# Optimization experiments

Hardware: AMD Instinct MI355X
Metric: run time of the kernel (lower is better)

Reference implementation:

```python
import jax, jax.numpy as jnp
import numpy as np

B, T, F_IN, H, L = 32, 2000, 80, 512, 2


def _ln(x, g, b, eps=1e-5):
    m = x.mean(-1, keepdims=True)
    v = x.var(-1, keepdims=True)
    return (x - m) / jnp.sqrt(v + eps) * g + b


def setup_inputs() -> dict:
    key = jax.random.key(0)
    ks = jax.random.split(key, 6)
    s = lambda k, shape, sc: jax.random.normal(k, shape, jnp.float32) * sc
    return {
        "x": s(ks[0], (B, T, F_IN), 1.0),
        "W_proj": s(ks[1], (F_IN, H), (1.0 / F_IN) ** 0.5),
        "b_proj": jnp.zeros((H,), jnp.float32),
        "ln1_g": jnp.ones((H,), jnp.float32),
        "ln1_b": jnp.zeros((H,), jnp.float32),
        "W_in": s(ks[2], (L, H, H), (1.0 / H) ** 0.5),
        "W_rec": s(ks[3], (L, H, H), (1.0 / H) ** 0.5),
        "b_rnn": jnp.zeros((L, H), jnp.float32),
        "tau_raw": jnp.ones((L, H), jnp.float32),
        "lno_g": jnp.ones((H,), jnp.float32),
        "lno_b": jnp.zeros((H,), jnp.float32),
    }


def _ltc_layer(x_tbh, W_i, W_r, b, tau_raw):
    # Liquid Time-Constant cell: tau*dh/dt = -h + tanh(Wx + Uh + b), dt = 1
    tau = jax.nn.softplus(tau_raw) + 0.1  # per-unit time constant, >0
    xz = jnp.einsum('tbf,fh->tbh', x_tbh, W_i) + b  # precompute input drive

    def step(h, xz_t):
        z = xz_t + h @ W_r
        h_new = h + (-h + jnp.tanh(z)) / tau
        return h_new, h_new

    h0 = jnp.zeros((x_tbh.shape[1], W_r.shape[0]), x_tbh.dtype)
    h_last, ys = jax.lax.scan(step, h0, xz)
    return ys, h_last


def reference(x, W_proj, b_proj, ln1_g, ln1_b, W_in, W_rec, b_rnn, tau_raw, lno_g, lno_b):
    # input projection: Linear -> LayerNorm -> GELU (dropout=0 in eval)
    h = jax.nn.gelu(_ln(x @ W_proj + b_proj, ln1_g, ln1_b), approximate=False)
    seq = jnp.transpose(h, (1, 0, 2))  # [T, B, H] for scan
    finals = []
    for l in range(W_in.shape[0]):
        seq, h_last = _ltc_layer(seq, W_in[l], W_rec[l], b_rnn[l], tau_raw[l])
        finals.append(h_last)
    encoded = _ln(jnp.transpose(seq, (1, 0, 2)), lno_g, lno_b)  # [B, T, H]
    hidden = jnp.stack(finals)  # [L, B, H]
    return encoded, hidden
```

## Files before the change

kernel.cpp:

```cpp
#include <hip/hip_runtime.h>
#include <math.h>

#define B_    32
#define T_    2000
#define FIN_  80
#define H_    512
#define ROWS_ (B_ * T_)
#define BTH_  ((size_t)ROWS_ * H_)
#define BH_   (B_ * H_)

typedef unsigned long long u64;

__global__ __launch_bounds__(256) void proj_ln_gelu(
    const float* __restrict__ x, const float* __restrict__ Wp,
    const float* __restrict__ bp, const float* __restrict__ g1,
    const float* __restrict__ be1, float* __restrict__ out)
{
  __shared__ float xs[16][84];
  __shared__ float pr[16][512];
  __shared__ float mv[16][2];
  const int tid = threadIdx.x;
  const int r0 = blockIdx.x * 16;

  for (int f = tid; f < 320; f += 256) {
    int rr = f / 20, c4 = (f % 20) * 4;
    int r = r0 + rr; int b = r & 31; int t = r >> 5;
    float4 v = *(const float4*)(x + ((size_t)(b * T_ + t)) * FIN_ + c4);
    xs[rr][c4+0] = v.x; xs[rr][c4+1] = v.y; xs[rr][c4+2] = v.z; xs[rr][c4+3] = v.w;
  }
  __syncthreads();

  const int j = tid;
  float acc0[16], acc1[16];
#pragma unroll
  for (int rr = 0; rr < 16; ++rr) { acc0[rr] = 0.f; acc1[rr] = 0.f; }

  for (int k4 = 0; k4 < 20; ++k4) {
    float w0[4], w1[4];
#pragma unroll
    for (int i = 0; i < 4; ++i) {
      w0[i] = Wp[(k4*4+i)*H_ + j];
      w1[i] = Wp[(k4*4+i)*H_ + j + 256];
    }
#pragma unroll
    for (int rr = 0; rr < 16; ++rr) {
      float4 xv = *(const float4*)&xs[rr][k4*4];
      acc0[rr] += xv.x*w0[0] + xv.y*w0[1] + xv.z*w0[2] + xv.w*w0[3];
      acc1[rr] += xv.x*w1[0] + xv.y*w1[1] + xv.z*w1[2] + xv.w*w1[3];
    }
  }

  const float bj0 = bp[j], bj1 = bp[j+256];
#pragma unroll
  for (int rr = 0; rr < 16; ++rr) {
    pr[rr][j]     = acc0[rr] + bj0;
    pr[rr][j+256] = acc1[rr] + bj1;
  }
  __syncthreads();

  const int wv = tid >> 6, ln = tid & 63;
  for (int rr = wv*4; rr < wv*4+4; ++rr) {
    float s = 0.f, ss = 0.f;
#pragma unroll
    for (int q = 0; q < 8; ++q) { float v = pr[rr][ln + q*64]; s += v; ss += v*v; }
#pragma unroll
    for (int o = 32; o > 0; o >>= 1) { s += __shfl_xor(s, o, 64); ss += __shfl_xor(ss, o, 64); }
    if (ln == 0) {
      float m = s * (1.f/512.f);
      float var = ss * (1.f/512.f) - m*m;
      mv[rr][0] = m; mv[rr][1] = 1.f / sqrtf(var + 1e-5f);
    }
  }
  __syncthreads();

  const float ga0 = g1[j], ga1 = g1[j+256], bo0 = be1[j], bo1 = be1[j+256];
#pragma unroll
  for (int rr = 0; rr < 16; ++rr) {
    float m = mv[rr][0], rs = mv[rr][1];
    float v0 = (pr[rr][j]     - m) * rs * ga0 + bo0;
    float v1 = (pr[rr][j+256] - m) * rs * ga1 + bo1;
    v0 = v0 * 0.5f * (1.f + erff(v0 * 0.70710678118654752f));
    v1 = v1 * 0.5f * (1.f + erff(v1 * 0.70710678118654752f));
    size_t ro = (size_t)(r0 + rr) * H_;
    out[ro + j] = v0; out[ro + j + 256] = v1;
  }
}

__global__ __launch_bounds__(256) void gemm512(
    const float* __restrict__ A, const float* __restrict__ Bm,
    const float* __restrict__ bias, float* __restrict__ C)
{
  __shared__ float As[16][132];
  __shared__ float Bs[16][132];
  const int tid = threadIdx.x;
  const int n0 = blockIdx.x * 128;
  const int m0 = blockIdx.y * 128;
  const int tx = tid & 15, ty = tid >> 4;

  float acc[8][8];
#pragma unroll
  for (int i = 0; i < 8; ++i)
#pragma unroll
    for (int jj = 0; jj < 8; ++jj) acc[i][jj] = 0.f;

  float4 pa[2], pb[2];
#pragma unroll
  for (int i = 0; i < 2; ++i) {
    int f = i*256 + tid;
    int mm = f >> 2, kk4 = (f & 3) * 4;
    pa[i] = *(const float4*)(A + (size_t)(m0+mm)*H_ + kk4);
    int kk = f >> 5, nn4 = (f & 31) * 4;
    pb[i] = *(const float4*)(Bm + (size_t)kk*H_ + n0 + nn4);
  }

  for (int kt = 0; kt < 32; ++kt) {
    __syncthreads();
#pragma unroll
    for (int i = 0; i < 2; ++i) {
      int f = i*256 + tid;
      int mm = f >> 2, kk4 = (f & 3) * 4;
      As[kk4+0][mm] = pa[i].x; As[kk4+1][mm] = pa[i].y;
      As[kk4+2][mm] = pa[i].z; As[kk4+3][mm] = pa[i].w;
      int kk = f >> 5, nn4 = (f & 31) * 4;
      *(float4*)&Bs[kk][nn4] = pb[i];
    }
    __syncthreads();
    if (kt < 31) {
#pragma unroll
      for (int i = 0; i < 2; ++i) {
        int f = i*256 + tid;
        int mm = f >> 2, kk4 = (f & 3) * 4;
        pa[i] = *(const float4*)(A + (size_t)(m0+mm)*H_ + (kt+1)*16 + kk4);
        int kk = f >> 5, nn4 = (f & 31) * 4;
        pb[i] = *(const float4*)(Bm + (size_t)((kt+1)*16+kk)*H_ + n0 + nn4);
      }
    }
#pragma unroll
    for (int k = 0; k < 16; ++k) {
      float a[8], bb[8];
      *(float4*)(a+0) = *(const float4*)&As[k][ty*4];
      *(float4*)(a+4) = *(const float4*)&As[k][ty*4 + 64];
      *(float4*)(bb+0) = *(const float4*)&Bs[k][tx*4];
      *(float4*)(bb+4) = *(const float4*)&Bs[k][tx*4 + 64];
#pragma unroll
      for (int i = 0; i < 8; ++i)
#pragma unroll
        for (int jj = 0; jj < 8; ++jj) acc[i][jj] += a[i] * bb[jj];
    }
  }

  float4 bi0 = *(const float4*)(bias + n0 + tx*4);
  float4 bi1 = *(const float4*)(bias + n0 + tx*4 + 64);
#pragma unroll
  for (int i = 0; i < 8; ++i) {
    int m = m0 + ty*4 + (i & 3) + (i >> 2) * 64;
    float4 v0 = make_float4(acc[i][0]+bi0.x, acc[i][1]+bi0.y, acc[i][2]+bi0.z, acc[i][3]+bi0.w);
    float4 v1 = make_float4(acc[i][4]+bi1.x, acc[i][5]+bi1.y, acc[i][6]+bi1.z, acc[i][7]+bi1.w);
    *(float4*)(C + (size_t)m*H_ + n0 + tx*4)      = v0;
    *(float4*)(C + (size_t)m*H_ + n0 + tx*4 + 64) = v1;
  }
}

__global__ __launch_bounds__(512) void ltc_scan(
    const float* __restrict__ Wrec,
    const float* __restrict__ traw,
    float* __restrict__ xzys,
    u64* __restrict__ hbuf,
    int* __restrict__ ctr,
    float* __restrict__ hid)
{
  __shared__ float hl[512];
  __shared__ float pt[32 * 64];
  __shared__ float taus[64];

  const int tid = threadIdx.x;
  const int b  = blockIdx.x & 31;
  const int s  = blockIdx.x >> 5;
  const int j0 = s * 64;
  const int cq = tid & 15;
  const int kg = tid >> 4;

  float wreg[64];
#pragma unroll
  for (int kk = 0; kk < 16; ++kk) {
    float4 wv = *(const float4*)(Wrec + (size_t)(kg*16 + kk)*H_ + j0 + cq*4);
    wreg[kk*4+0] = wv.x; wreg[kk*4+1] = wv.y; wreg[kk*4+2] = wv.z; wreg[kk*4+3] = wv.w;
  }
  if (tid < 64) {
    float tr = traw[j0 + tid];
    taus[tid] = (tr > 20.f ? tr : log1pf(expf(tr))) + 0.1f;
  }
  int* cb = ctr + b * 16;
  __syncthreads();

  for (int t = 0; t < T_; ++t) {
    if (t > 0) {
      if (tid == 0) {
        const int want = 8 * t;
        while (__hip_atomic_load(cb, __ATOMIC_RELAXED, __HIP_MEMORY_SCOPE_AGENT) < want) {
          __builtin_amdgcn_s_sleep(1);
        }
      }
      __syncthreads();
      const u64* hrd = hbuf + (size_t)((t - 1) & 1) * (B_ * 256) + b * 256;
      if (tid < 256) {
        u64 v = __hip_atomic_load(hrd + tid, __ATOMIC_RELAXED, __HIP_MEMORY_SCOPE_AGENT);
        union { u64 u; float f[2]; } cv; cv.u = v;
        hl[tid*2]   = cv.f[0];
        hl[tid*2+1] = cv.f[1];
      }
    } else {
      if (tid < 128) *(float4*)(hl + tid*4) = make_float4(0.f, 0.f, 0.f, 0.f);
    }
    float2 xzv = make_float2(0.f, 0.f);
    if (tid < 32)
      xzv = *(const float2*)(xzys + ((size_t)t * B_ + b) * H_ + j0 + tid*2);
    __syncthreads();

    float hr[16];
#pragma unroll
    for (int q = 0; q < 4; ++q)
      *(float4*)(hr + q*4) = *(const float4*)(hl + kg*16 + q*4);

    float a0 = 0.f, a1 = 0.f, a2 = 0.f, a3 = 0.f;
#pragma unroll
    for (int kk = 0; kk < 16; ++kk) {
      float h = hr[kk];
      a0 += h * wreg[kk*4+0]; a1 += h * wreg[kk*4+1];
      a2 += h * wreg[kk*4+2]; a3 += h * wreg[kk*4+3];
    }
    *(float4*)(pt + kg*64 + cq*4) = make_float4(a0, a1, a2, a3);
    __syncthreads();

    if (tid < 32) {
      float s0 = 0.f, s1 = 0.f;
#pragma unroll
      for (int g = 0; g < 32; ++g) {
        float2 p = *(const float2*)(pt + g*64 + tid*2);
        s0 += p.x; s1 += p.y;
      }
      float z0 = xzv.x + s0, z1 = xzv.y + s1;
      float th0 = tanhf(z0), th1 = tanhf(z1);
      float h0 = hl[j0 + tid*2], h1 = hl[j0 + tid*2 + 1];
      float hn0 = h0 + (th0 - h0) / taus[tid*2];
      float hn1 = h1 + (th1 - h1) / taus[tid*2 + 1];
      *(float2*)(xzys + ((size_t)t * B_ + b) * H_ + j0 + tid*2) = make_float2(hn0, hn1);
      union { u64 u; float f[2]; } cv; cv.f[0] = hn0; cv.f[1] = hn1;
      u64* hw = hbuf + (size_t)(t & 1) * (B_ * 256) + b * 256 + s * 32 + tid;
      __hip_atomic_store(hw, cv.u, __ATOMIC_RELAXED, __HIP_MEMORY_SCOPE_AGENT);
      if (t == T_ - 1)
        *(float2*)(hid + b*H_ + j0 + tid*2) = make_float2(hn0, hn1);
    }
    if (tid == 0) {
      asm volatile("s_waitcnt vmcnt(0)" ::: "memory");
      __hip_atomic_fetch_add(cb, 1, __ATOMIC_RELAXED, __HIP_MEMORY_SCOPE_AGENT);
    }
  }
}

__global__ __launch_bounds__(256) void ln_out(
    const float* __restrict__ in, const float* __restrict__ g,
    const float* __restrict__ be, float* __restrict__ out)
{
  __shared__ float red[8];
  __shared__ float mv2[2];
  const int r = blockIdx.x;
  const int t = r >> 5, b = r & 31;
  const int tid = threadIdx.x;

  const float2 v = *(const float2*)(in + (size_t)r * H_ + tid*2);
  float s = v.x + v.y, ss = v.x*v.x + v.y*v.y;
#pragma unroll
  for (int o = 32; o > 0; o >>= 1) { s += __shfl_xor(s, o, 64); ss += __shfl_xor(ss, o, 64); }
  const int wv = tid >> 6;
  if ((tid & 63) == 0) { red[wv] = s; red[4 + wv] = ss; }
  __syncthreads();
  if (tid == 0) {
    float S  = red[0] + red[1] + red[2] + red[3];
    float SS = red[4] + red[5] + red[6] + red[7];
    float m = S * (1.f/512.f);
    mv2[0] = m;
    mv2[1] = 1.f / sqrtf(SS * (1.f/512.f) - m*m + 1e-5f);
  }
  __syncthreads();
  const float m = mv2[0], rs = mv2[1];
  const float2 gg = *(const float2*)(g + tid*2);
  const float2 bb = *(const float2*)(be + tid*2);
  float2 o2;
  o2.x = (v.x - m) * rs * gg.x + bb.x;
  o2.y = (v.y - m) * rs * gg.y + bb.y;
  *(float2*)(out + ((size_t)b * T_ + t) * H_ + tid*2) = o2;
}

extern "C" void kernel_launch(void* const* d_in, const int* in_sizes, int n_in,
                              void* d_out, int out_size, void* d_ws, size_t ws_size,
                              hipStream_t stream)
{
  (void)in_sizes; (void)n_in; (void)out_size; (void)ws_size;
  const float* x   = (const float*)d_in[0];
  const float* Wp  = (const float*)d_in[1];
  const float* bp  = (const float*)d_in[2];
  const float* g1  = (const float*)d_in[3];
  const float* be1 = (const float*)d_in[4];
  const float* Win = (const float*)d_in[5];
  const float* Wrc = (const float*)d_in[6];
  const float* brn = (const float*)d_in[7];
  const float* tra = (const float*)d_in[8];
  const float* gno = (const float*)d_in[9];
  const float* bno = (const float*)d_in[10];
  float* outp = (float*)d_out;

  char* ws = (char*)d_ws;
  int*  ctr  = (int*)ws;
  u64*  hbuf = (u64*)(ws + 4096);
  float* bufA = (float*)(ws + 4096 + 131072);

  proj_ln_gelu<<<dim3(ROWS_/16), 256, 0, stream>>>(x, Wp, bp, g1, be1, bufA);

  gemm512<<<dim3(4, ROWS_/128), 256, 0, stream>>>(bufA, Win, brn, outp);

  hipMemsetAsync(ctr, 0, 32 * 16 * sizeof(int), stream);
  ltc_scan<<<256, 512, 0, stream>>>(Wrc, tra, outp, hbuf, ctr, outp + BTH_);

  gemm512<<<dim3(4, ROWS_/128), 256, 0, stream>>>(outp, Win + H_*H_, brn + H_, bufA);

  hipMemsetAsync(ctr, 0, 32 * 16 * sizeof(int), stream);
  ltc_scan<<<256, 512, 0, stream>>>(Wrc + H_*H_, tra + H_, bufA, hbuf, ctr,
                                    outp + BTH_ + BH_);

  ln_out<<<ROWS_, 256, 0, stream>>>(bufA, gno, bno, outp);
}
```

Baseline: 10.00 ms.

## Fuse both LTC layers and output LayerNorm into one pipelined persistent scan

Replaces the two sequential scan kernels, the middle GEMM and the output LayerNorm with one persistent kernel. The first 256 blocks run layer 0, and 512 more blocks run layer 1 one step behind, computing the input projection on the fly with W_in and W_rec held in registers and writing the normalized output directly. Synchronisation uses per-element tags carrying the step number plus per-timestep bitmask flags instead of a counter. The aim is to overlap the two recurrences and drop a full GEMM pass and an LN pass. In exchange it relies on all 768 blocks being resident at once, and when workspace is small it falls back to using the input x buffer as sync scratch.

```diff
diff --git a/kernel.cpp b/kernel.cpp
--- a/kernel.cpp
+++ b/kernel.cpp
@@ -10,6 +10,7 @@
 #define BH_   (B_ * H_)
 
 typedef unsigned long long u64;
+typedef unsigned int u32;
 
 __global__ __launch_bounds__(256) void proj_ln_gelu(
     const float* __restrict__ x, const float* __restrict__ Wp,
@@ -161,142 +162,256 @@
   }
 }
 
-__global__ __launch_bounds__(512) void ltc_scan(
-    const float* __restrict__ Wrec,
-    const float* __restrict__ traw,
-    float* __restrict__ xzys,
-    u64* __restrict__ hbuf,
-    int* __restrict__ ctr,
-    float* __restrict__ hid)
+__global__ __launch_bounds__(512, 6) void fused_scan(
+    const float* __restrict__ Wrc0,
+    const float* __restrict__ Win1,
+    const float* __restrict__ Wrc1,
+    const float* __restrict__ tra,
+    const float* __restrict__ brn1,
+    const float* __restrict__ lng, const float* __restrict__ lnb,
+    float* __restrict__ bufA,
+    u64* __restrict__ h0tag,
+    u64* __restrict__ h1tag,
+    u32* __restrict__ ysflag,
+    float* __restrict__ enc,
+    float* __restrict__ hid0,
+    float* __restrict__ hid1)
 {
-  __shared__ float hl[512];
-  __shared__ float pt[32 * 64];
-  __shared__ float taus[64];
-
+  __shared__ float hl[1024];
+  __shared__ float pt[2048];
   const int tid = threadIdx.x;
-  const int b  = blockIdx.x & 31;
-  const int s  = blockIdx.x >> 5;
-  const int j0 = s * 64;
-  const int cq = tid & 15;
-  const int kg = tid >> 4;
-
-  float wreg[64];
-#pragma unroll
-  for (int kk = 0; kk < 16; ++kk) {
-    float4 wv = *(const float4*)(Wrec + (size_t)(kg*16 + kk)*H_ + j0 + cq*4);
-    wreg[kk*4+0] = wv.x; wreg[kk*4+1] = wv.y; wreg[kk*4+2] = wv.z; wreg[kk*4+3] = wv.w;
-  }
-  if (tid < 64) {
-    float tr = traw[j0 + tid];
-    taus[tid] = (tr > 20.f ? tr : log1pf(expf(tr))) + 0.1f;
-  }
-  int* cb = ctr + b * 16;
-  __syncthreads();
-
-  for (int t = 0; t < T_; ++t) {
-    if (t > 0) {
+
+  if (blockIdx.x < 256) {
+    const int b  = blockIdx.x & 31;
+    const int s  = blockIdx.x >> 5;
+    const int j0 = s * 64;
+    const int kg = tid >> 4;
+    const int cq = tid & 15;
+
+    float wreg[64];
+#pragma unroll
+    for (int kk = 0; kk < 16; ++kk) {
+      float4 wv = *(const float4*)(Wrc0 + (size_t)(kg*16 + kk)*H_ + j0 + cq*4);
+      wreg[kk*4+0] = wv.x; wreg[kk*4+1] = wv.y; wreg[kk*4+2] = wv.z; wreg[kk*4+3] = wv.w;
+    }
+    float tau0 = 1.f, tau1 = 1.f;
+    if (tid < 32) {
+      float tr0 = tra[j0 + 2*tid], tr1 = tra[j0 + 2*tid + 1];
+      tau0 = (tr0 > 20.f ? tr0 : log1pf(expf(tr0))) + 0.1f;
+      tau1 = (tr1 > 20.f ? tr1 : log1pf(expf(tr1))) + 0.1f;
+    }
+    __syncthreads();
+
+    for (int t = 0; t < T_; ++t) {
+      float2 xzv = make_float2(0.f, 0.f);
+      if (tid < 32)
+        xzv = *(const float2*)(bufA + ((size_t)t * B_ + b) * H_ + j0 + 2*tid);
+
+      if (t > 0) {
+        const u64* rb = h0tag + ((size_t)((t + 1) & 1) * B_ + b) * H_;
+        u64 v = __hip_atomic_load(rb + tid, __ATOMIC_RELAXED, __HIP_MEMORY_SCOPE_AGENT);
+        while ((u32)(v >> 32) != (u32)t) {
+          __builtin_amdgcn_s_sleep(1);
+          v = __hip_atomic_load(rb + tid, __ATOMIC_RELAXED, __HIP_MEMORY_SCOPE_AGENT);
+        }
+        hl[tid] = __uint_as_float((u32)v);
+      } else {
+        hl[tid] = 0.f;
+      }
+      __syncthreads();
+
+      float hr[16];
+#pragma unroll
+      for (int q = 0; q < 4; ++q)
+        *(float4*)(hr + q*4) = *(const float4*)(hl + kg*16 + q*4);
+      float a0 = 0.f, a1 = 0.f, a2 = 0.f, a3 = 0.f;
+#pragma unroll
+      for (int kk = 0; kk < 16; ++kk) {
+        float h = hr[kk];
+        a0 += h * wreg[kk*4+0]; a1 += h * wreg[kk*4+1];
+        a2 += h * wreg[kk*4+2]; a3 += h * wreg[kk*4+3];
+      }
+      *(float4*)&pt[kg*64 + cq*4] = make_float4(a0, a1, a2, a3);
+      __syncthreads();
+
+      if (tid < 64) {
+        int c2 = tid & 31;
+        float s0 = 0.f, s1 = 0.f;
+        for (int g = tid >> 5; g < 32; g += 2) {
+          float2 p = *(const float2*)&pt[g*64 + c2*2];
+          s0 += p.x; s1 += p.y;
+        }
+        s0 += __shfl_xor(s0, 32, 64);
+        s1 += __shfl_xor(s1, 32, 64);
+        if (tid < 32) {
+          float z0 = xzv.x + s0, z1 = xzv.y + s1;
+          float th0 = tanhf(z0), th1 = tanhf(z1);
+          float h0v = hl[j0 + 2*tid], h1v = hl[j0 + 2*tid + 1];
+          float hn0 = h0v + (th0 - h0v) / tau0;
+          float hn1 = h1v + (th1 - h1v) / tau1;
+          u64* wb = h0tag + ((size_t)(t & 1) * B_ + b) * H_ + j0 + 2*tid;
+          u64 tg = ((u64)(u32)(t + 1)) << 32;
+          __hip_atomic_store(wb,     tg | __float_as_uint(hn0), __ATOMIC_RELAXED, __HIP_MEMORY_SCOPE_AGENT);
+          __hip_atomic_store(wb + 1, tg | __float_as_uint(hn1), __ATOMIC_RELAXED, __HIP_MEMORY_SCOPE_AGENT);
+          union { u64 u; float f[2]; } cv; cv.f[0] = hn0; cv.f[1] = hn1;
+          u64* yw = (u64*)bufA + (((size_t)t * B_ + b) * H_ + j0) / 2 + tid;
+          __hip_atomic_store(yw, cv.u, __ATOMIC_RELAXED, __HIP_MEMORY_SCOPE_AGENT);
+          if (t == T_ - 1)
+            *(float2*)(hid0 + b*H_ + j0 + 2*tid) = make_float2(hn0, hn1);
+        }
+      }
       if (tid == 0) {
-        const int want = 8 * t;
-        while (__hip_atomic_load(cb, __ATOMIC_RELAXED, __HIP_MEMORY_SCOPE_AGENT) < want) {
+        asm volatile("s_waitcnt vmcnt(0)" ::: "memory");
+        __hip_atomic_fetch_or(ysflag + (size_t)t * B_ + b, 1u << s,
+                              __ATOMIC_RELAXED, __HIP_MEMORY_SCOPE_AGENT);
+      }
+      __syncthreads();
+    }
+  } else {
+    const int idx = blockIdx.x - 256;
+    const int b  = idx >> 4;
+    const int s  = idx & 15;
+    const int j0 = s * 32;
+    const int kg = tid >> 3;
+    const int cq = tid & 7;
+
+    float wreg[64];
+#pragma unroll
+    for (int kk = 0; kk < 16; ++kk) {
+      const float* base = (kg < 32)
+          ? (Win1 + (size_t)(kg*16 + kk)*H_)
+          : (Wrc1 + (size_t)((kg - 32)*16 + kk)*H_);
+      float4 wv = *(const float4*)(base + j0 + cq*4);
+      wreg[kk*4+0] = wv.x; wreg[kk*4+1] = wv.y; wreg[kk*4+2] = wv.z; wreg[kk*4+3] = wv.w;
+    }
+    float tauc = 1.f, bic = 0.f, gc = 1.f, bcc = 0.f;
+    if (tid < 32) {
+      float tr = tra[H_ + j0 + tid];
+      tauc = (tr > 20.f ? tr : log1pf(expf(tr))) + 0.1f;
+      bic = brn1[j0 + tid];
+      gc = lng[j0 + tid];
+      bcc = lnb[j0 + tid];
+    }
+    __syncthreads();
+
+    for (int t = 0; t < T_; ++t) {
+      if (tid == 0) {
+        while (__hip_atomic_load(ysflag + (size_t)t * B_ + b,
+                                 __ATOMIC_RELAXED, __HIP_MEMORY_SCOPE_AGENT) != 0xFFu)
           __builtin_amdgcn_s_sleep(1);
-        }
-      }
-      __syncthreads();
-      const u64* hrd = hbuf + (size_t)((t - 1) & 1) * (B_ * 256) + b * 256;
+      }
+      __syncthreads();
+
+      const u64* rb = h1tag + ((size_t)((t + 1) & 1) * B_ + b) * H_;
+      u64 hv = 0;
+      if (t > 0)
+        hv = __hip_atomic_load(rb + tid, __ATOMIC_RELAXED, __HIP_MEMORY_SCOPE_AGENT);
       if (tid < 256) {
-        u64 v = __hip_atomic_load(hrd + tid, __ATOMIC_RELAXED, __HIP_MEMORY_SCOPE_AGENT);
-        union { u64 u; float f[2]; } cv; cv.u = v;
-        hl[tid*2]   = cv.f[0];
-        hl[tid*2+1] = cv.f[1];
-      }
-    } else {
-      if (tid < 128) *(float4*)(hl + tid*4) = make_float4(0.f, 0.f, 0.f, 0.f);
-    }
-    float2 xzv = make_float2(0.f, 0.f);
-    if (tid < 32)
-      xzv = *(const float2*)(xzys + ((size_t)t * B_ + b) * H_ + j0 + tid*2);
-    __syncthreads();
-
-    float hr[16];
-#pragma unroll
-    for (int q = 0; q < 4; ++q)
-      *(float4*)(hr + q*4) = *(const float4*)(hl + kg*16 + q*4);
-
-    float a0 = 0.f, a1 = 0.f, a2 = 0.f, a3 = 0.f;
-#pragma unroll
-    for (int kk = 0; kk < 16; ++kk) {
-      float h = hr[kk];
-      a0 += h * wreg[kk*4+0]; a1 += h * wreg[kk*4+1];
-      a2 += h * wreg[kk*4+2]; a3 += h * wreg[kk*4+3];
-    }
-    *(float4*)(pt + kg*64 + cq*4) = make_float4(a0, a1, a2, a3);
-    __syncthreads();
-
-    if (tid < 32) {
-      float s0 = 0.f, s1 = 0.f;
-#pragma unroll
-      for (int g = 0; g < 32; ++g) {
-        float2 p = *(const float2*)(pt + g*64 + tid*2);
-        s0 += p.x; s1 += p.y;
-      }
-      float z0 = xzv.x + s0, z1 = xzv.y + s1;
-      float th0 = tanhf(z0), th1 = tanhf(z1);
-      float h0 = hl[j0 + tid*2], h1 = hl[j0 + tid*2 + 1];
-      float hn0 = h0 + (th0 - h0) / taus[tid*2];
-      float hn1 = h1 + (th1 - h1) / taus[tid*2 + 1];
-      *(float2*)(xzys + ((size_t)t * B_ + b) * H_ + j0 + tid*2) = make_float2(hn0, hn1);
-      union { u64 u; float f[2]; } cv; cv.f[0] = hn0; cv.f[1] = hn1;
-      u64* hw = hbuf + (size_t)(t & 1) * (B_ * 256) + b * 256 + s * 32 + tid;
-      __hip_atomic_store(hw, cv.u, __ATOMIC_RELAXED, __HIP_MEMORY_SCOPE_AGENT);
-      if (t == T_ - 1)
-        *(float2*)(hid + b*H_ + j0 + tid*2) = make_float2(hn0, hn1);
-    }
-    if (tid == 0) {
-      asm volatile("s_waitcnt vmcnt(0)" ::: "memory");
-      __hip_atomic_fetch_add(cb, 1, __ATOMIC_RELAXED, __HIP_MEMORY_SCOPE_AGENT);
-    }
-  }
-}
-
-__global__ __launch_bounds__(256) void ln_out(
-    const float* __restrict__ in, const float* __restrict__ g,
-    const float* __restrict__ be, float* __restrict__ out)
-{
-  __shared__ float red[8];
-  __shared__ float mv2[2];
-  const int r = blockIdx.x;
-  const int t = r >> 5, b = r & 31;
-  const int tid = threadIdx.x;
-
-  const float2 v = *(const float2*)(in + (size_t)r * H_ + tid*2);
-  float s = v.x + v.y, ss = v.x*v.x + v.y*v.y;
-#pragma unroll
-  for (int o = 32; o > 0; o >>= 1) { s += __shfl_xor(s, o, 64); ss += __shfl_xor(ss, o, 64); }
-  const int wv = tid >> 6;
-  if ((tid & 63) == 0) { red[wv] = s; red[4 + wv] = ss; }
-  __syncthreads();
-  if (tid == 0) {
-    float S  = red[0] + red[1] + red[2] + red[3];
-    float SS = red[4] + red[5] + red[6] + red[7];
-    float m = S * (1.f/512.f);
-    mv2[0] = m;
-    mv2[1] = 1.f / sqrtf(SS * (1.f/512.f) - m*m + 1e-5f);
-  }
-  __syncthreads();
-  const float m = mv2[0], rs = mv2[1];
-  const float2 gg = *(const float2*)(g + tid*2);
-  const float2 bb = *(const float2*)(be + tid*2);
-  float2 o2;
-  o2.x = (v.x - m) * rs * gg.x + bb.x;
-  o2.y = (v.y - m) * rs * gg.y + bb.y;
-  *(float2*)(out + ((size_t)b * T_ + t) * H_ + tid*2) = o2;
+        u64 yv = __hip_atomic_load((const u64*)bufA + ((size_t)t * B_ + b) * (H_/2) + tid,
+                                   __ATOMIC_RELAXED, __HIP_MEMORY_SCOPE_AGENT);
+        union { u64 u; float f[2]; } cv; cv.u = yv;
+        hl[2*tid]     = cv.f[0];
+        hl[2*tid + 1] = cv.f[1];
+      }
+      if (t > 0) {
+        while ((u32)(hv >> 32) != (u32)t) {
+          __builtin_amdgcn_s_sleep(1);
+          hv = __hip_atomic_load(rb + tid, __ATOMIC_RELAXED, __HIP_MEMORY_SCOPE_AGENT);
+        }
+        hl[512 + tid] = __uint_as_float((u32)hv);
+      } else {
+        hl[512 + tid] = 0.f;
+      }
+      __syncthreads();
+
+      float hr[16];
+#pragma unroll
+      for (int q = 0; q < 4; ++q)
+        *(float4*)(hr + q*4) = *(const float4*)(hl + kg*16 + q*4);
+      float a0 = 0.f, a1 = 0.f, a2 = 0.f, a3 = 0.f;
+#pragma unroll
+      for (int kk = 0; kk < 16; ++kk) {
+        float h = hr[kk];
+        a0 += h * wreg[kk*4+0]; a1 += h * wreg[kk*4+1];
+        a2 += h * wreg[kk*4+2]; a3 += h * wreg[kk*4+3];
+      }
+      *(float4*)&pt[kg*32 + cq*4] = make_float4(a0, a1, a2, a3);
+      __syncthreads();
+
+      if (tid < 64) {
+        int c = tid & 31;
+        float ps = 0.f;
+        for (int g = tid >> 5; g < 64; g += 2) ps += pt[g*32 + c];
+        ps += __shfl_xor(ps, 32, 64);
+        float hn = 0.f, hold = 0.f;
+        if (tid < 32) {
+          float z = ps + bic;
+          float th = tanhf(z);
+          hold = hl[512 + j0 + tid];
+          hn = hold + (th - hold) / tauc;
+          u64* wb = h1tag + ((size_t)(t & 1) * B_ + b) * H_ + j0 + tid;
+          __hip_atomic_store(wb, (((u64)(u32)(t + 1)) << 32) | __float_as_uint(hn),
+                             __ATOMIC_RELAXED, __HIP_MEMORY_SCOPE_AGENT);
+          if (t == T_ - 1) hid1[b*H_ + j0 + tid] = hn;
+        }
+        if (t > 0) {
+          float sm = 0.f, ss = 0.f;
+#pragma unroll
+          for (int q = 0; q < 8; ++q) {
+            float v = hl[512 + tid*8 + q];
+            sm += v; ss += v*v;
+          }
+#pragma unroll
+          for (int o = 32; o > 0; o >>= 1) {
+            sm += __shfl_xor(sm, o, 64);
+            ss += __shfl_xor(ss, o, 64);
+          }
+          float m = sm * (1.f/512.f);
+          float rs = 1.f / sqrtf(ss * (1.f/512.f) - m*m + 1e-5f);
+          if (tid < 32)
+            enc[((size_t)b * T_ + (t - 1)) * H_ + j0 + tid] = (hold - m) * rs * gc + bcc;
+        }
+      }
+      __syncthreads();
+    }
+
+    {
+      const u64* rb = h1tag + ((size_t)((T_ - 1) & 1) * B_ + b) * H_;
+      u64 v = __hip_atomic_load(rb + tid, __ATOMIC_RELAXED, __HIP_MEMORY_SCOPE_AGENT);
+      while ((u32)(v >> 32) != (u32)T_) {
+        __builtin_amdgcn_s_sleep(1);
+        v = __hip_atomic_load(rb + tid, __ATOMIC_RELAXED, __HIP_MEMORY_SCOPE_AGENT);
+      }
+      hl[512 + tid] = __uint_as_float((u32)v);
+      __syncthreads();
+      if (tid < 64) {
+        float sm = 0.f, ss = 0.f;
+#pragma unroll
+        for (int q = 0; q < 8; ++q) {
+          float vv = hl[512 + tid*8 + q];
+          sm += vv; ss += vv*vv;
+        }
+#pragma unroll
+        for (int o = 32; o > 0; o >>= 1) {
+          sm += __shfl_xor(sm, o, 64);
+          ss += __shfl_xor(ss, o, 64);
+        }
+        float m = sm * (1.f/512.f);
+        float rs = 1.f / sqrtf(ss * (1.f/512.f) - m*m + 1e-5f);
+        if (tid < 32) {
+          float hold = hl[512 + j0 + tid];
+          enc[((size_t)b * T_ + (T_ - 1)) * H_ + j0 + tid] = (hold - m) * rs * gc + bcc;
+        }
+      }
+    }
+  }
 }
 
 extern "C" void kernel_launch(void* const* d_in, const int* in_sizes, int n_in,
                               void* d_out, int out_size, void* d_ws, size_t ws_size,
                               hipStream_t stream)
 {
-  (void)in_sizes; (void)n_in; (void)out_size; (void)ws_size;
+  (void)in_sizes; (void)n_in; (void)out_size;
   const float* x   = (const float*)d_in[0];
   const float* Wp  = (const float*)d_in[1];
   const float* bp  = (const float*)d_in[2];
@@ -310,23 +425,33 @@
   const float* bno = (const float*)d_in[10];
   float* outp = (float*)d_out;
 
-  char* ws = (char*)d_ws;
-  int*  ctr  = (int*)ws;
-  u64*  hbuf = (u64*)(ws + 4096);
-  float* bufA = (float*)(ws + 4096 + 131072);
-
-  proj_ln_gelu<<<dim3(ROWS_/16), 256, 0, stream>>>(x, Wp, bp, g1, be1, bufA);
-
-  gemm512<<<dim3(4, ROWS_/128), 256, 0, stream>>>(bufA, Win, brn, outp);
-
-  hipMemsetAsync(ctr, 0, 32 * 16 * sizeof(int), stream);
-  ltc_scan<<<256, 512, 0, stream>>>(Wrc, tra, outp, hbuf, ctr, outp + BTH_);
-
-  gemm512<<<dim3(4, ROWS_/128), 256, 0, stream>>>(outp, Win + H_*H_, brn + H_, bufA);
-
-  hipMemsetAsync(ctr, 0, 32 * 16 * sizeof(int), stream);
-  ltc_scan<<<256, 512, 0, stream>>>(Wrc + H_*H_, tra + H_, bufA, hbuf, ctr,
-                                    outp + BTH_ + BH_);
-
-  ln_out<<<ROWS_, 256, 0, stream>>>(bufA, gno, bno, outp);
+  const size_t H0T_BYTES = (size_t)2 * B_ * H_ * 8;
+  const size_t YSF_BYTES = (size_t)T_ * B_ * 4;
+  const size_t SYNC_BYTES = 786432;
+  const size_t BUFA_BYTES = BTH_ * 4;
+
+  char* sync;
+  float* bufA;
+  if (ws_size >= SYNC_BYTES + BUFA_BYTES) {
+    sync = (char*)d_ws;
+    bufA = (float*)((char*)d_ws + SYNC_BYTES);
+  } else {
+    sync = (char*)d_in[0];
+    bufA = (float*)d_ws;
+  }
+  u64* h0tag  = (u64*)sync;
+  u64* h1tag  = (u64*)(sync + H0T_BYTES);
+  u32* ysflag = (u32*)(sync + 2 * H0T_BYTES);
+  (void)YSF_BYTES;
+
+  proj_ln_gelu<<<dim3(ROWS_/16), 256, 0, stream>>>(x, Wp, bp, g1, be1, outp);
+
+  gemm512<<<dim3(4, ROWS_/128), 256, 0, stream>>>(outp, Win, brn, bufA);
+
+  hipMemsetAsync(sync, 0, SYNC_BYTES, stream);
+
+  fused_scan<<<768, 512, 0, stream>>>(
+      Wrc, Win + H_*H_, Wrc + H_*H_, tra, brn + H_, gno, bno,
+      bufA, h0tag, h1tag, ysflag,
+      outp, outp + BTH_, outp + BTH_ + BH_);
 }
```

Result: slower. 11.35 ms (+13.4%).
